# Kernel tuning notes

Measured on AMD Instinct MI355X. Metric: run time of the kernel, lower is better.

Reference implementation:

```python
import jax, jax.numpy as jnp
import numpy as np

N_NODES = 50000
N_EDGES = 800000
GEN_EPS = 1e-7
LN_EPS = 1e-5


def _mlp3_tanh(x, w0, b0, w1, b1, w2, b2):
    x = jnp.tanh(x @ w0.T + b0)
    x = jnp.tanh(x @ w1.T + b1)
    return jnp.tanh(x @ w2.T + b2)


def _gen_conv(x, src, dst, edge_attr, w0, b0, ln_w, ln_b, w1, b1):
    # GENConv(aggr='softmax', t=1): msg = relu(x_j + e) + eps
    msg = jax.nn.relu(x[src] + edge_attr) + GEN_EPS          # [E, 64]
    m = jax.ops.segment_max(msg, dst, num_segments=N_NODES)  # [N, 64]
    ex = jnp.exp(msg - m[dst])
    den = jax.ops.segment_sum(ex, dst, num_segments=N_NODES)
    alpha = ex / den[dst]                                    # scatter-softmax per dst
    agg = jax.ops.segment_sum(alpha * msg, dst, num_segments=N_NODES)
    h = x + agg                                              # x_r + aggregated messages
    # internal MLP: Linear(64->128), LayerNorm(128), ReLU, Linear(128->64)
    h = h @ w0.T + b0
    mu = jnp.mean(h, axis=-1, keepdims=True)
    var = jnp.mean((h - mu) ** 2, axis=-1, keepdims=True)
    h = ln_w * (h - mu) * jax.lax.rsqrt(var + LN_EPS) + ln_b
    h = jax.nn.relu(h)
    return h @ w1.T + b1


def setup_inputs() -> dict:
    key = jax.random.key(0)
    ks = jax.random.split(key, 32)
    s = 0.05
    d = {
        'node_features': jax.random.normal(ks[0], (N_NODES, 11), jnp.float32),
        'edge_features': jax.random.normal(ks[1], (N_EDGES, 3), jnp.float32),
        'edge_index': jax.random.randint(ks[2], (2, N_EDGES), 0, N_NODES, jnp.int32),
        'ne_w0': jax.random.normal(ks[3], (64, 11)) * s, 'ne_b0': jnp.zeros((64,)),
        'ne_w1': jax.random.normal(ks[4], (64, 64)) * s, 'ne_b1': jnp.zeros((64,)),
        'ne_w2': jax.random.normal(ks[5], (64, 64)) * s, 'ne_b2': jnp.zeros((64,)),
        'ee_w0': jax.random.normal(ks[6], (64, 3)) * s, 'ee_b0': jnp.zeros((64,)),
        'ee_w1': jax.random.normal(ks[7], (64, 64)) * s, 'ee_b1': jnp.zeros((64,)),
        'ee_w2': jax.random.normal(ks[8], (64, 64)) * s, 'ee_b2': jnp.zeros((64,)),
        'mp_w0': jax.random.normal(ks[9], (3, 128, 64)) * s,
        'mp_b0': jnp.zeros((3, 128)),
        'mp_ln_w': jnp.ones((3, 128)), 'mp_ln_b': jnp.zeros((3, 128)),
        'mp_w1': jax.random.normal(ks[10], (3, 64, 128)) * s,
        'mp_b1': jnp.zeros((3, 64)),
        'pi_w0': jax.random.normal(ks[11], (64, 64)) * s, 'pi_b0': jnp.zeros((64,)),
        'pi_w1': jax.random.normal(ks[12], (64, 64)) * s, 'pi_b1': jnp.zeros((64,)),
        'pi_w2': jax.random.normal(ks[13], (2, 64)) * s, 'pi_b2': jnp.zeros((2,)),
    }
    return {k: (v.astype(jnp.float32) if v.dtype != jnp.int32 else v) for k, v in d.items()}


def reference(node_features, edge_features, edge_index,
              ne_w0, ne_b0, ne_w1, ne_b1, ne_w2, ne_b2,
              ee_w0, ee_b0, ee_w1, ee_b1, ee_w2, ee_b2,
              mp_w0, mp_b0, mp_ln_w, mp_ln_b, mp_w1, mp_b1,
              pi_w0, pi_b0, pi_w1, pi_b1, pi_w2, pi_b2):
    src, dst = edge_index[0], edge_index[1]
    x = _mlp3_tanh(node_features, ne_w0, ne_b0, ne_w1, ne_b1, ne_w2, ne_b2)
    e = _mlp3_tanh(edge_features, ee_w0, ee_b0, ee_w1, ee_b1, ee_w2, ee_b2)
    for i in range(3):
        x = _gen_conv(x, src, dst, e, mp_w0[i], mp_b0[i], mp_ln_w[i], mp_ln_b[i], mp_w1[i], mp_b1[i])
    h = jnp.tanh(x @ pi_w0.T + pi_b0)
    h = jnp.tanh(h @ pi_w1.T + pi_b1)
    out = h @ pi_w2.T + pi_b2                 # [N, 2]
    # output.t().reshape(-1)[:n_turbines] == first column of out
    means = -30.0 + (out[:, 0] + 1.0) * 60.0 / 2.0
    return means
```

## Files before the change

kernel.cpp:

```cpp
#include <hip/hip_runtime.h>
#include <stdint.h>

#define N_NODES 50000
#define N_EDGES 800000

typedef unsigned short u16;
typedef unsigned int u32;
typedef __attribute__((ext_vector_type(8))) short short8;
typedef __attribute__((ext_vector_type(4))) float f32x4;
typedef __attribute__((ext_vector_type(4))) u32 u32x4;
typedef __attribute__((ext_vector_type(2))) u32 u32x2;

#define WAVE_SYNC() asm volatile("s_waitcnt lgkmcnt(0)" ::: "memory")

__device__ __forceinline__ float b2f(u16 v) {
    u32 u = ((u32)v) << 16; float f; __builtin_memcpy(&f, &u, 4); return f;
}
__device__ __forceinline__ u16 f2b(float f) {
    u32 u; __builtin_memcpy(&u, &f, 4);
    return (u16)((u + 0x8000u) >> 16);
}
__device__ __forceinline__ float lo2f(u32 p) {
    u32 u = p << 16; float f; __builtin_memcpy(&f, &u, 4); return f;
}
__device__ __forceinline__ float hi2f(u32 p) {
    u32 u = p & 0xffff0000u; float f; __builtin_memcpy(&f, &u, 4); return f;
}
__device__ __forceinline__ u32 pack2(float a, float b) {
    u32 ua, ub; __builtin_memcpy(&ua, &a, 4); __builtin_memcpy(&ub, &b, 4);
    return __builtin_amdgcn_perm(ub + 0x8000u, ua + 0x8000u, 0x07060302u);
}
__device__ __forceinline__ f32x4 mfma16(short8 a, short8 b, f32x4 c) {
    return __builtin_amdgcn_mfma_f32_16x16x32_bf16(a, b, c, 0, 0, 0);
}

#define TANH_TBL_N 192
__device__ __forceinline__ void build_tanh_tbl(float2* tbl) {
    int i = (int)threadIdx.x;
    if (i < TANH_TBL_N) {
        float x0 = i * 0.03125f, x1 = x0 + 0.03125f;
        float t0 = tanhf(x0), t1 = tanhf(x1);
        float s = (t1 - t0) * 32.f;
        tbl[i] = make_float2(fmaf(-s, x0, t0), s);
    }
    __syncthreads();
}
__device__ __forceinline__ float lut_tanh(const float2* __restrict__ tbl, float x) {
    float a = __builtin_fabsf(x);
    a = fminf(a, 5.96875f);
    int i = (int)(a * 32.f);
    float2 bs = tbl[i];
    float y = fmaf(bs.y, a, bs.x);
    return copysignf(y, x);
}

enum : int {
    NE_T0 = 0,     NE_B0 = 704,   NE_T1 = 768,   NE_B1 = 4864,  NE_T2 = 4928,  NE_B2 = 9024,
    EE_T0 = 9088,  EE_B0 = 9280,  EE_T1 = 9344,  EE_B1 = 13440, EE_T2 = 13504, EE_B2 = 17600,
    MP_T0 = 17664, MP_B0 = 42240, LNW_O = 42624, LNB_O = 43008, MP_T1 = 43392, MP_B1 = 67968,
    PI_T0 = 68160, PI_B0 = 72256, PI_T1 = 72320, PI_B1 = 76416, PI_W2 = 76480, PI_B2 = 76608,
    W_TOTAL = 76610
};

enum : int {
    FR_EE1 = 0, FR_EE2 = 4, FR_EE3 = 12, FR_NE1 = 20, FR_NE2 = 24, FR_NE3 = 32,
    FR_MP0 = 40, FR_MP1 = 88, FR_PI0 = 136, FR_PI1 = 144, FR_TOTAL = 152
};

#define OFF_W       ((size_t)0)
#define OFF_FLAG    ((size_t)0x60000)
#define OFF_WB      ((size_t)0x61000)
#define OFF_XB0     ((size_t)0x90000)
#define OFF_XB1     ((size_t)0x700000)
#define OFF_H64B    ((size_t)0xE00000)
#define OFF_E       ((size_t)0x1500000)
#define OFF_ROWPTR  ((size_t)0x8300000)
#define OFF_CURSOR  ((size_t)0x8340000)
#define OFF_CNT     ((size_t)0x8380000)
#define OFF_PERM    ((size_t)0x83C0000)
#define OFF_SRCS    ((size_t)0x8700000)
#define OFF_BSUM    ((size_t)0x8A80000)

struct Ptrs24 { const void* p[24]; };


__global__ void detect_kernel(const void* nf, int* flag) {
    u32 w = ((const u32*)nf)[threadIdx.x & 63];
    u32 lo = w & 0xffffu;
    int e = (int)((lo >> 7) & 0xff);
    int good = ((e >= 118 && e <= 132) || lo == 0) ? 1 : 0;
    unsigned long long b = __ballot(good != 0);
    if (threadIdx.x == 0) *flag = (__popcll(b) >= 48) ? 1 : 0;
}

__global__ void convert_weights(Ptrs24 ps, float* __restrict__ W, const int* flag) {
    const int segIN[24] = {11,64,64,64,64,64, 3,64,64,64,64,64, 64,384,384,384,128,192, 64,64,64,64,128,2};
    const int segOUT[24]= {64, 1,64, 1,64, 1, 64, 1,64, 1,64, 1, 128, 1,  1,  1, 64,  1, 64, 1,64, 1,  1,1};
    const int segS[24]  = { 1, 1, 1, 1, 1, 1,  1, 1, 1, 1, 1, 1,   3, 1,  1,  1,  3,  1,  1, 1, 1, 1,  1,1};
    const int segTR[24] = { 1, 0, 1, 0, 1, 0,  1, 0, 1, 0, 1, 0,   1, 0,  0,  0,  1,  0,  1, 0, 1, 0,  0,0};
    int t = blockIdx.x * blockDim.x + threadIdx.x;
    if (t >= W_TOTAL) return;
    bool bf = (*flag != 0);
    int seg = 0, off = t;
    for (;;) {
        int cnt = segIN[seg] * segOUT[seg] * segS[seg];
        if (off < cnt) break;
        off -= cnt; seg++;
    }
    int srcIdx;
    if (segTR[seg]) {
        int per = segIN[seg] * segOUT[seg];
        int s = off / per, d = off % per;
        int j = d / segOUT[seg], i = d % segOUT[seg];
        srcIdx = s * per + i * segIN[seg] + j;
    } else {
        srcIdx = off;
    }
    const void* p = ps.p[seg];
    W[t] = bf ? b2f(((const u16*)p)[srcIdx]) : ((const float*)p)[srcIdx];
}

__global__ void make_frags(const float* __restrict__ W, u16* __restrict__ Wb) {
    const int base[15] = {FR_EE1,FR_EE2,FR_EE3,FR_NE1,FR_NE2,FR_NE3,
                          FR_MP0,FR_MP0+16,FR_MP0+32, FR_MP1,FR_MP1+16,FR_MP1+32,
                          FR_PI0,FR_PI1,FR_TOTAL};
    const int woff[14] = {EE_T0,EE_T1,EE_T2, NE_T0,NE_T1,NE_T2,
                          MP_T0,MP_T0+8192,MP_T0+16384, MP_T1,MP_T1+8192,MP_T1+16384,
                          PI_T0,PI_T1};
    const int kreal[14] = {3,64,64, 11,64,64, 64,64,64, 128,128,128, 64,64};
    const int nn[14]    = {64,64,64, 64,64,64, 128,128,128, 64,64,64, 64,64};
    int t = blockIdx.x * blockDim.x + threadIdx.x;
    if (t >= FR_TOTAL * 512) return;
    int f = t >> 9, r = t & 511, lane = r >> 3, j = r & 7;
    int l = 0;
    while (f >= base[l + 1]) l++;
    int lf = f - base[l];
    int NT = nn[l] >> 4;
    int kt = lf / NT, nt = lf % NT;
    int k = kt * 32 + (lane >> 4) * 8 + j;
    int n = nt * 16 + (lane & 15);
    float v = (k < kreal[l]) ? W[woff[l] + k * nn[l] + n] : 0.f;
    u32 u; __builtin_memcpy(&u, &v, 4);
    Wb[t] = (u16)((u + 0x7fffu + ((u >> 16) & 1u)) >> 16);
}


__global__ void hist_kernel(const int* __restrict__ dst, int* __restrict__ cnts) {
    int e = blockIdx.x * blockDim.x + threadIdx.x;
    if (e < N_EDGES) atomicAdd(&cnts[dst[e]], 1);
}

__global__ void scanA(const int* __restrict__ cnts, int* __restrict__ prow,
                      int* __restrict__ bsum) {
    __shared__ int wsum[16];
    int tid = threadIdx.x, lane = tid & 63, wid = tid >> 6;
    int i0 = blockIdx.x * 2048 + tid * 2;
    int v0 = 0, v1 = 0;
    if (i0 >= 1 && i0 <= N_NODES) v0 = (cnts[i0 - 1] + 1) & ~1;
    if (i0 + 1 <= N_NODES && i0 + 1 >= 1) v1 = (cnts[i0] + 1) & ~1;
    int v = v0 + v1;
#pragma unroll
    for (int off = 1; off < 64; off <<= 1) {
        int t = __shfl_up(v, off, 64);
        if (lane >= off) v += t;
    }
    if (lane == 63) wsum[wid] = v;
    __syncthreads();
    if (tid == 0) { int a = 0; for (int w = 0; w < 16; w++) { a += wsum[w]; wsum[w] = a; } }
    __syncthreads();
    int incl = v + (wid ? wsum[wid - 1] : 0);
    if (i0 <= N_NODES) prow[i0] = incl - v1;
    if (i0 + 1 <= N_NODES) prow[i0 + 1] = incl;
    if (tid == 1023) bsum[blockIdx.x] = incl;
}
__global__ void scanB(int* __restrict__ bsum, int nb) {
    int lane = threadIdx.x;
    int v = (lane < nb) ? bsum[lane] : 0;
#pragma unroll
    for (int off = 1; off < 64; off <<= 1) {
        int t = __shfl_up(v, off, 64);
        if (lane >= off) v += t;
    }
    if (lane < nb) bsum[lane] = v;
}
__global__ void scanC(const int* __restrict__ bsum, int* __restrict__ prow,
                      int* __restrict__ cursor) {
    int i = blockIdx.x * 1024 + threadIdx.x;
    if (i > N_NODES) return;
    int b = i >> 11;
    int v = prow[i] + (b ? bsum[b - 1] : 0);
    prow[i] = v;
    if (i < N_NODES) cursor[i] = v;
}

__global__ void scatter_kernel(const int* __restrict__ dst, const int* __restrict__ src,
                               int* __restrict__ cursor, int* __restrict__ perm,
                               int* __restrict__ srcs) {
    int e = blockIdx.x * blockDim.x + threadIdx.x;
    if (e >= N_EDGES) return;
    int p = atomicAdd(&cursor[dst[e]], 1);
    perm[e] = p;
    srcs[p] = src[e];
}


template<int KT, int NT, int INSTR>
__device__ __forceinline__ void mfma_layer(const u32* ldsin, int lane,
        const short8* __restrict__ Wf, int basef, const float* __restrict__ bias, f32x4* acc) {
    int q = lane >> 4, mr = lane & 15;
#pragma unroll
    for (int nt = 0; nt < NT; nt++) acc[nt] = *(const f32x4*)(bias + nt * 16 + q * 4);
#pragma unroll
    for (int kt = 0; kt < KT; kt++) {
        short8 act = *(const short8*)(ldsin + mr * INSTR + kt * 16 + q * 4);
#pragma unroll
        for (int nt = 0; nt < NT; nt++)
            acc[nt] = mfma16(Wf[(basef + kt * NT + nt) * 64 + lane], act, acc[nt]);
    }
}

template<int KT, int NT>
__device__ __forceinline__ void mfma_layer_reg(const short8* act, int lane,
        const short8* __restrict__ Wf, int basef, const float* __restrict__ bias, f32x4* acc) {
    int q = lane >> 4;
#pragma unroll
    for (int nt = 0; nt < NT; nt++) acc[nt] = *(const f32x4*)(bias + nt * 16 + q * 4);
#pragma unroll
    for (int kt = 0; kt < KT; kt++)
#pragma unroll
        for (int nt = 0; nt < NT; nt++)
            acc[nt] = mfma16(Wf[(basef + kt * NT + nt) * 64 + lane], act[kt], acc[nt]);
}

template<int NT, int OUTSTR>
__device__ __forceinline__ void tanh_pack_lds(const f32x4* acc, u32* ldsout, int lane,
                                              const float2* __restrict__ tbl) {
    int q = lane >> 4, mr = lane & 15;
#pragma unroll
    for (int nt = 0; nt < NT; nt++) {
        f32x4 a = acc[nt];
        ldsout[mr * OUTSTR + nt * 8 + q * 2 + 0] = pack2(lut_tanh(tbl, a[0]), lut_tanh(tbl, a[1]));
        ldsout[mr * OUTSTR + nt * 8 + q * 2 + 1] = pack2(lut_tanh(tbl, a[2]), lut_tanh(tbl, a[3]));
    }
}


__global__ __launch_bounds__(256) void edge_encoder(const void* ef, u32* __restrict__ ebuf,
        const int* __restrict__ perm, const float* __restrict__ W,
        const short8* __restrict__ Wf, const int* flag) {
    __shared__ u32 lds[4 * 1152];
    __shared__ float2 tbl[TANH_TBL_N];
    build_tanh_tbl(tbl);
    int wv = threadIdx.x >> 6, lane = threadIdx.x & 63;
    u32* B0 = lds + wv * 1152;
    u32* B1 = B0 + 576;
    long ebase = (long)blockIdx.x * 64 + wv * 16;
    bool bf = (*flag != 0);
    if (lane < 16) {
        long e = ebase + lane;
        float i0, i1, i2;
        if (bf) { const u16* p = (const u16*)ef + e * 3; i0 = b2f(p[0]); i1 = b2f(p[1]); i2 = b2f(p[2]); }
        else    { const float* p = (const float*)ef + e * 3; i0 = p[0]; i1 = p[1]; i2 = p[2]; }
        u32* row = B0 + lane * 36;
        row[0] = pack2(i0, i1); row[1] = pack2(i2, 0.f);
#pragma unroll
        for (int d = 2; d < 16; d++) row[d] = 0;
    }
    WAVE_SYNC();
    f32x4 acc[4];
    mfma_layer<1, 4, 36>(B0, lane, Wf, FR_EE1, W + EE_B0, acc);
    tanh_pack_lds<4, 36>(acc, B1, lane, tbl);
    WAVE_SYNC();
    mfma_layer<2, 4, 36>(B1, lane, Wf, FR_EE2, W + EE_B1, acc);
    tanh_pack_lds<4, 36>(acc, B0, lane, tbl);
    WAVE_SYNC();
    mfma_layer<2, 4, 36>(B0, lane, Wf, FR_EE3, W + EE_B2, acc);
    tanh_pack_lds<4, 36>(acc, B1, lane, tbl);
    WAVE_SYNC();
    int ro = lane >> 2, cc = (lane & 3) * 8;
    long e = ebase + ro;
    long prowp = perm[e];
    u32x4 v0 = *(const u32x4*)&B1[ro * 36 + cc];
    u32x4 v1 = *(const u32x4*)&B1[ro * 36 + cc + 4];
    *(u32x4*)&ebuf[prowp * 32 + cc] = v0;
    *(u32x4*)&ebuf[prowp * 32 + cc + 4] = v1;
}

__global__ __launch_bounds__(256) void node_encoder(const void* nf,
        u16* __restrict__ xbf, const float* __restrict__ W,
        const short8* __restrict__ Wf, const int* flag) {
    __shared__ u32 lds[4 * 1152];
    __shared__ float2 tbl[TANH_TBL_N];
    build_tanh_tbl(tbl);
    int wv = threadIdx.x >> 6, lane = threadIdx.x & 63;
    int q = lane >> 4, mr = lane & 15;
    u32* B0 = lds + wv * 1152;
    u32* B1 = B0 + 576;
    long nbase = (long)blockIdx.x * 64 + wv * 16;
    bool bf = (*flag != 0);
    if (lane < 16) {
        long n = nbase + lane;
        float in[12];
#pragma unroll
        for (int j = 0; j < 12; j++) in[j] = 0.f;
        if (n < N_NODES) {
#pragma unroll
            for (int j = 0; j < 11; j++)
                in[j] = bf ? b2f(((const u16*)nf)[n * 11 + j]) : ((const float*)nf)[n * 11 + j];
        }
        u32* row = B0 + lane * 36;
#pragma unroll
        for (int d = 0; d < 6; d++) row[d] = pack2(in[2 * d], in[2 * d + 1]);
#pragma unroll
        for (int d = 6; d < 16; d++) row[d] = 0;
    }
    WAVE_SYNC();
    f32x4 acc[4];
    mfma_layer<1, 4, 36>(B0, lane, Wf, FR_NE1, W + NE_B0, acc);
    tanh_pack_lds<4, 36>(acc, B1, lane, tbl);
    WAVE_SYNC();
    mfma_layer<2, 4, 36>(B1, lane, Wf, FR_NE2, W + NE_B1, acc);
    tanh_pack_lds<4, 36>(acc, B0, lane, tbl);
    WAVE_SYNC();
    mfma_layer<2, 4, 36>(B0, lane, Wf, FR_NE3, W + NE_B2, acc);
    long n = nbase + mr;
    if (n < N_NODES) {
#pragma unroll
        for (int nt = 0; nt < 4; nt++) {
            float v0 = lut_tanh(tbl, acc[nt][0]), v1 = lut_tanh(tbl, acc[nt][1]);
            float v2 = lut_tanh(tbl, acc[nt][2]), v3 = lut_tanh(tbl, acc[nt][3]);
            u32x2 pb; pb.x = pack2(v0, v1); pb.y = pack2(v2, v3);
            *(u32x2*)&xbf[n * 64 + nt * 16 + q * 4] = pb;
        }
    }
}

__global__ __launch_bounds__(256) void aggregate_kernel(
        const u32* __restrict__ xbf32, const u32* __restrict__ ebuf32,
        const int* __restrict__ srcs, const int* __restrict__ prow,
        u32* __restrict__ h64bf32) {
    int wid = (int)((blockIdx.x * 256 + threadIdx.x) >> 6);
    int lane = (int)(threadIdx.x & 63);
    int n0 = __builtin_amdgcn_readfirstlane(wid) * 4;
    if (n0 >= N_NODES) return;
    int half = lane >> 5, h = lane & 31;
    int rl = n0 + (lane < 4 ? lane : 4);
    if (rl > N_NODES) rl = N_NODES;
    int rv = prow[rl];
    int win = __shfl(rv, 0, 64);
    int sk = srcs[win + lane];
    for (int j = 0; j < 4; j++) {
        int n = n0 + j;
        if (n >= N_NODES) break;
        int kb = __shfl(rv, j, 64);
        int ke = __shfl(rv, j + 1, 64);
        u32 xr = xbf32[(long)n * 32 + h];
        float num0 = 0.f, den0 = 0.f, num1 = 0.f, den1 = 0.f;
        for (int k = kb; k < ke; k += 2) {
            if (k + 1 >= win + 64) { win = k; sk = srcs[win + lane]; }
            int s = __shfl(sk, k - win + half, 64);
            u32 ev = ebuf32[(long)(k + half) * 32 + h];
            bool valid = s >= 0;
            long sr = valid ? (long)s : 0;
            u32 xv = xbf32[sr * 32 + h];
            float m0 = fmaxf(lo2f(xv) + lo2f(ev), 0.f) + 1e-7f;
            float m1 = fmaxf(hi2f(xv) + hi2f(ev), 0.f) + 1e-7f;
            float w0 = valid ? __expf(m0) : 0.f;
            float w1 = valid ? __expf(m1) : 0.f;
            num0 = fmaf(w0, m0, num0); den0 += w0;
            num1 = fmaf(w1, m1, num1); den1 += w1;
        }
        num0 += __shfl_xor(num0, 32, 64); den0 += __shfl_xor(den0, 32, 64);
        num1 += __shfl_xor(num1, 32, 64); den1 += __shfl_xor(den1, 32, 64);
        if (half == 0) {
            float agg0 = (den0 > 0.f) ? __fdividef(num0, den0) : 0.f;
            float agg1 = (den1 > 0.f) ? __fdividef(num1, den1) : 0.f;
            h64bf32[(long)n * 32 + h] = pack2(lo2f(xr) + agg0, hi2f(xr) + agg1);
        }
    }
}

__global__ __launch_bounds__(256) void mlp_fused(const u16* __restrict__ h64bf,
        u16* __restrict__ xbf,
        const float* __restrict__ W, const short8* __restrict__ Wf, int r) {
    __shared__ u32 lds[4 * 1088];
    int wv = threadIdx.x >> 6, lane = threadIdx.x & 63;
    int q = lane >> 4, mr = lane & 15;
    u32* bufY = lds + wv * 1088;
    long nbase = (long)blockIdx.x * 64 + wv * 16;
    long row = nbase + mr;
    long rc = (row < N_NODES) ? row : (N_NODES - 1);
    short8 act[2];
#pragma unroll
    for (int kt = 0; kt < 2; kt++)
        act[kt] = *(const short8*)&h64bf[rc * 64 + kt * 32 + q * 8];
    f32x4 acc[8];
    mfma_layer_reg<2, 8>(act, lane, Wf, FR_MP0 + r * 16, W + MP_B0 + r * 128, acc);
    float s = 0.f, sq = 0.f;
#pragma unroll
    for (int nt = 0; nt < 8; nt++)
#pragma unroll
        for (int rr = 0; rr < 4; rr++) { float v = acc[nt][rr]; s += v; sq = fmaf(v, v, sq); }
    s += __shfl_xor(s, 16, 64);  s += __shfl_xor(s, 32, 64);
    sq += __shfl_xor(sq, 16, 64); sq += __shfl_xor(sq, 32, 64);
    float mu = s * (1.f / 128.f);
    float var = sq * (1.f / 128.f) - mu * mu;
    float inv = rsqrtf(var + 1e-5f);
    const float* LW = W + LNW_O + r * 128;
    const float* LB = W + LNB_O + r * 128;
#pragma unroll
    for (int nt = 0; nt < 8; nt++) {
        f32x4 lw = *(const f32x4*)(LW + nt * 16 + q * 4);
        f32x4 lb = *(const f32x4*)(LB + nt * 16 + q * 4);
        float u0 = fmaxf(fmaf((acc[nt][0] - mu) * inv, lw[0], lb[0]), 0.f);
        float u1 = fmaxf(fmaf((acc[nt][1] - mu) * inv, lw[1], lb[1]), 0.f);
        float u2 = fmaxf(fmaf((acc[nt][2] - mu) * inv, lw[2], lb[2]), 0.f);
        float u3 = fmaxf(fmaf((acc[nt][3] - mu) * inv, lw[3], lb[3]), 0.f);
        bufY[mr * 68 + nt * 8 + q * 2 + 0] = pack2(u0, u1);
        bufY[mr * 68 + nt * 8 + q * 2 + 1] = pack2(u2, u3);
    }
    WAVE_SYNC();
    f32x4 acc2[4];
    mfma_layer<4, 4, 68>(bufY, lane, Wf, FR_MP1 + r * 16, W + MP_B1 + r * 64, acc2);
    if (row < N_NODES) {
#pragma unroll
        for (int nt = 0; nt < 4; nt++) {
            f32x4 v = acc2[nt];
            u32x2 pb; pb.x = pack2(v[0], v[1]); pb.y = pack2(v[2], v[3]);
            *(u32x2*)&xbf[row * 64 + nt * 16 + q * 4] = pb;
        }
    }
}

__global__ __launch_bounds__(256) void policy_head(const u16* __restrict__ xbf, void* out,
        const float* __restrict__ W, const short8* __restrict__ Wf, const int* flag) {
    __shared__ u32 lds[4 * 576];
    __shared__ float2 tbl[TANH_TBL_N];
    build_tanh_tbl(tbl);
    int wv = threadIdx.x >> 6, lane = threadIdx.x & 63;
    int q = lane >> 4, mr = lane & 15;
    u32* bufY = lds + wv * 576;
    long nbase = (long)blockIdx.x * 64 + wv * 16;
    long row = nbase + mr;
    long rc = (row < N_NODES) ? row : (N_NODES - 1);
    bool bf = (*flag != 0);
    short8 act[2];
#pragma unroll
    for (int kt = 0; kt < 2; kt++)
        act[kt] = *(const short8*)&xbf[rc * 64 + kt * 32 + q * 8];
    f32x4 acc[4];
    mfma_layer_reg<2, 4>(act, lane, Wf, FR_PI0, W + PI_B0, acc);
    tanh_pack_lds<4, 36>(acc, bufY, lane, tbl);
    WAVE_SYNC();
    mfma_layer<2, 4, 36>(bufY, lane, Wf, FR_PI1, W + PI_B1, acc);
    float o = 0.f;
#pragma unroll
    for (int nt = 0; nt < 4; nt++) {
        f32x4 w2 = *(const f32x4*)(W + PI_W2 + nt * 16 + q * 4);
#pragma unroll
        for (int rr = 0; rr < 4; rr++) o = fmaf(lut_tanh(tbl, acc[nt][rr]), w2[rr], o);
    }
    o += __shfl_xor(o, 16, 64);
    o += __shfl_xor(o, 32, 64);
    if (lane < 16 && row < N_NODES) {
        float means = 30.f * (o + W[PI_B2]);
        if (bf) ((u16*)out)[row] = f2b(means);
        else    ((float*)out)[row] = means;
    }
}

extern "C" void kernel_launch(void* const* d_in, const int* in_sizes, int n_in,
                              void* d_out, int out_size, void* d_ws, size_t ws_size,
                              hipStream_t stream) {
    char* ws = (char*)d_ws;
    float* W      = (float*)(ws + OFF_W);
    int*   flag   = (int*)(ws + OFF_FLAG);
    u16*   Wb     = (u16*)(ws + OFF_WB);
    const short8* Wf = (const short8*)(ws + OFF_WB);
    u16*   xb0    = (u16*)(ws + OFF_XB0);
    u16*   xb1    = (u16*)(ws + OFF_XB1);
    u16*   h64bf  = (u16*)(ws + OFF_H64B);
    u32*   h64b32 = (u32*)(ws + OFF_H64B);
    u32*   ebuf32 = (u32*)(ws + OFF_E);
    int*   prow   = (int*)(ws + OFF_ROWPTR);
    int*   cursor = (int*)(ws + OFF_CURSOR);
    int*   cnts   = (int*)(ws + OFF_CNT);
    int*   perm   = (int*)(ws + OFF_PERM);
    int*   srcs   = (int*)(ws + OFF_SRCS);
    int*   bsum   = (int*)(ws + OFF_BSUM);

    const int* ei   = (const int*)d_in[2];
    const int* srcv = ei;
    const int* dstv = ei + N_EDGES;

    detect_kernel<<<1, 64, 0, stream>>>(d_in[0], flag);
    hipMemsetAsync(cnts, 0, N_NODES * sizeof(int), stream);
    hipMemsetAsync(srcs, 0xFF, (size_t)0x340000, stream);

    Ptrs24 ps;
    for (int k = 0; k < 24; k++) ps.p[k] = d_in[3 + k];
    convert_weights<<<(W_TOTAL + 255) / 256, 256, 0, stream>>>(ps, W, flag);
    make_frags<<<(FR_TOTAL * 512 + 255) / 256, 256, 0, stream>>>(W, Wb);

    hist_kernel<<<(N_EDGES + 255) / 256, 256, 0, stream>>>(dstv, cnts);
    scanA<<<25, 1024, 0, stream>>>(cnts, prow, bsum);
    scanB<<<1, 64, 0, stream>>>(bsum, 25);
    scanC<<<(N_NODES + 1024) / 1024, 1024, 0, stream>>>(bsum, prow, cursor);
    scatter_kernel<<<(N_EDGES + 255) / 256, 256, 0, stream>>>(dstv, srcv, cursor, perm, srcs);

    node_encoder<<<(N_NODES + 63) / 64, 256, 0, stream>>>(d_in[0], xb0, W, Wf, flag);
    edge_encoder<<<N_EDGES / 64, 256, 0, stream>>>(d_in[1], ebuf32, perm, W, Wf, flag);

    u16* xbc = xb0; u16* xbn = xb1;
    const int aggBlocks = ((N_NODES + 3) / 4 * 64 + 255) / 256;
    for (int r = 0; r < 3; r++) {
        aggregate_kernel<<<aggBlocks, 256, 0, stream>>>(
            (const u32*)xbc, ebuf32, srcs, prow, h64b32);
        mlp_fused<<<(N_NODES + 63) / 64, 256, 0, stream>>>(h64bf, xbn, W, Wf, r);
        u16* tb = xbc; xbc = xbn; xbn = tb;
    }
    policy_head<<<(N_NODES + 63) / 64, 256, 0, stream>>>(xbc, d_out, W, Wf, flag);
}
```

Baseline: 461.9 us.

## Restructure aggregation to two nodes per wave; precompute tanh table once; drop scanB

Each aggregate wave now handles 2 destination nodes instead of 4. It stages 64-edge windows of source indices in LDS and walks a shared window for both nodes, instead of reloading a register window and shuffling. The tanh lookup table is now built once in make_frags and copied into LDS by each kernel, so blocks no longer call tanhf. scanB is removed by having scanC sum the preceding block totals in a loop, and encoder LDS zeroing is spread across all lanes. These target per-node serialisation, launch count and redundant transcendental work. In exchange there are more waves for aggregation and extra LDS syncs.

After: 431.9 us. -6.5%, faster.

```diff
diff --git a/kernel.cpp b/kernel.cpp
--- a/kernel.cpp
+++ b/kernel.cpp
@@ -35,14 +35,9 @@
 }
 
 #define TANH_TBL_N 192
-__device__ __forceinline__ void build_tanh_tbl(float2* tbl) {
+__device__ __forceinline__ void load_tbl(const float2* __restrict__ g, float2* tbl) {
     int i = (int)threadIdx.x;
-    if (i < TANH_TBL_N) {
-        float x0 = i * 0.03125f, x1 = x0 + 0.03125f;
-        float t0 = tanhf(x0), t1 = tanhf(x1);
-        float s = (t1 - t0) * 32.f;
-        tbl[i] = make_float2(fmaf(-s, x0, t0), s);
-    }
+    if (i < TANH_TBL_N) tbl[i] = g[i];
     __syncthreads();
 }
 __device__ __forceinline__ float lut_tanh(const float2* __restrict__ tbl, float x) {
@@ -70,6 +65,7 @@
 #define OFF_W       ((size_t)0)
 #define OFF_FLAG    ((size_t)0x60000)
 #define OFF_WB      ((size_t)0x61000)
+#define OFF_TBL     ((size_t)0x88000)
 #define OFF_XB0     ((size_t)0x90000)
 #define OFF_XB1     ((size_t)0x700000)
 #define OFF_H64B    ((size_t)0xE00000)
@@ -120,7 +116,8 @@
     W[t] = bf ? b2f(((const u16*)p)[srcIdx]) : ((const float*)p)[srcIdx];
 }
 
-__global__ void make_frags(const float* __restrict__ W, u16* __restrict__ Wb) {
+__global__ void make_frags(const float* __restrict__ W, u16* __restrict__ Wb,
+                           float2* __restrict__ gtbl) {
     const int base[15] = {FR_EE1,FR_EE2,FR_EE3,FR_NE1,FR_NE2,FR_NE3,
                           FR_MP0,FR_MP0+16,FR_MP0+32, FR_MP1,FR_MP1+16,FR_MP1+32,
                           FR_PI0,FR_PI1,FR_TOTAL};
@@ -130,7 +127,16 @@
     const int kreal[14] = {3,64,64, 11,64,64, 64,64,64, 128,128,128, 64,64};
     const int nn[14]    = {64,64,64, 64,64,64, 128,128,128, 64,64,64, 64,64};
     int t = blockIdx.x * blockDim.x + threadIdx.x;
-    if (t >= FR_TOTAL * 512) return;
+    if (t >= FR_TOTAL * 512) {
+        int i = t - FR_TOTAL * 512;
+        if (i < TANH_TBL_N) {
+            float x0 = i * 0.03125f, x1 = x0 + 0.03125f;
+            float t0 = tanhf(x0), t1 = tanhf(x1);
+            float s = (t1 - t0) * 32.f;
+            gtbl[i] = make_float2(fmaf(-s, x0, t0), s);
+        }
+        return;
+    }
     int f = t >> 9, r = t & 511, lane = r >> 3, j = r & 7;
     int l = 0;
     while (f >= base[l + 1]) l++;
@@ -173,22 +179,14 @@
     if (i0 + 1 <= N_NODES) prow[i0 + 1] = incl;
     if (tid == 1023) bsum[blockIdx.x] = incl;
 }
-__global__ void scanB(int* __restrict__ bsum, int nb) {
-    int lane = threadIdx.x;
-    int v = (lane < nb) ? bsum[lane] : 0;
-#pragma unroll
-    for (int off = 1; off < 64; off <<= 1) {
-        int t = __shfl_up(v, off, 64);
-        if (lane >= off) v += t;
-    }
-    if (lane < nb) bsum[lane] = v;
-}
 __global__ void scanC(const int* __restrict__ bsum, int* __restrict__ prow,
                       int* __restrict__ cursor) {
     int i = blockIdx.x * 1024 + threadIdx.x;
     if (i > N_NODES) return;
-    int b = i >> 11;
-    int v = prow[i] + (b ? bsum[b - 1] : 0);
+    int nb = (int)(blockIdx.x >> 1);
+    int add = 0;
+    for (int b = 0; b < nb; b++) add += bsum[b];
+    int v = prow[i] + add;
     prow[i] = v;
     if (i < N_NODES) cursor[i] = v;
 }
@@ -244,18 +242,27 @@
     }
 }
 
+__device__ __forceinline__ void zero_stage(u32* B0, int lane) {
+#pragma unroll
+    for (int it = 0; it < 4; it++) {
+        int f = lane + 64 * it;
+        B0[(f >> 4) * 36 + (f & 15)] = 0;
+    }
+}
+
 
 __global__ __launch_bounds__(256) void edge_encoder(const void* ef, u32* __restrict__ ebuf,
         const int* __restrict__ perm, const float* __restrict__ W,
-        const short8* __restrict__ Wf, const int* flag) {
+        const short8* __restrict__ Wf, const float2* __restrict__ gtbl, const int* flag) {
     __shared__ u32 lds[4 * 1152];
     __shared__ float2 tbl[TANH_TBL_N];
-    build_tanh_tbl(tbl);
+    load_tbl(gtbl, tbl);
     int wv = threadIdx.x >> 6, lane = threadIdx.x & 63;
     u32* B0 = lds + wv * 1152;
     u32* B1 = B0 + 576;
     long ebase = (long)blockIdx.x * 64 + wv * 16;
     bool bf = (*flag != 0);
+    zero_stage(B0, lane);
     if (lane < 16) {
         long e = ebase + lane;
         float i0, i1, i2;
@@ -263,8 +270,6 @@
         else    { const float* p = (const float*)ef + e * 3; i0 = p[0]; i1 = p[1]; i2 = p[2]; }
         u32* row = B0 + lane * 36;
         row[0] = pack2(i0, i1); row[1] = pack2(i2, 0.f);
-#pragma unroll
-        for (int d = 2; d < 16; d++) row[d] = 0;
     }
     WAVE_SYNC();
     f32x4 acc[4];
@@ -288,31 +293,29 @@
 
 __global__ __launch_bounds__(256) void node_encoder(const void* nf,
         u16* __restrict__ xbf, const float* __restrict__ W,
-        const short8* __restrict__ Wf, const int* flag) {
+        const short8* __restrict__ Wf, const float2* __restrict__ gtbl, const int* flag) {
     __shared__ u32 lds[4 * 1152];
     __shared__ float2 tbl[TANH_TBL_N];
-    build_tanh_tbl(tbl);
+    load_tbl(gtbl, tbl);
     int wv = threadIdx.x >> 6, lane = threadIdx.x & 63;
     int q = lane >> 4, mr = lane & 15;
     u32* B0 = lds + wv * 1152;
     u32* B1 = B0 + 576;
     long nbase = (long)blockIdx.x * 64 + wv * 16;
     bool bf = (*flag != 0);
+    zero_stage(B0, lane);
     if (lane < 16) {
         long n = nbase + lane;
-        float in[12];
-#pragma unroll
-        for (int j = 0; j < 12; j++) in[j] = 0.f;
         if (n < N_NODES) {
+            float in[11];
 #pragma unroll
             for (int j = 0; j < 11; j++)
                 in[j] = bf ? b2f(((const u16*)nf)[n * 11 + j]) : ((const float*)nf)[n * 11 + j];
-        }
-        u32* row = B0 + lane * 36;
-#pragma unroll
-        for (int d = 0; d < 6; d++) row[d] = pack2(in[2 * d], in[2 * d + 1]);
-#pragma unroll
-        for (int d = 6; d < 16; d++) row[d] = 0;
+            u32* row = B0 + lane * 36;
+#pragma unroll
+            for (int d = 0; d < 5; d++) row[d] = pack2(in[2 * d], in[2 * d + 1]);
+            row[5] = pack2(in[10], 0.f);
+        }
     }
     WAVE_SYNC();
     f32x4 acc[4];
@@ -339,43 +342,65 @@
         const u32* __restrict__ xbf32, const u32* __restrict__ ebuf32,
         const int* __restrict__ srcs, const int* __restrict__ prow,
         u32* __restrict__ h64bf32) {
+    __shared__ int ldsW[4][64];
+    int wv = threadIdx.x >> 6;
     int wid = (int)((blockIdx.x * 256 + threadIdx.x) >> 6);
     int lane = (int)(threadIdx.x & 63);
-    int n0 = __builtin_amdgcn_readfirstlane(wid) * 4;
+    int n0 = __builtin_amdgcn_readfirstlane(wid) * 2;
     if (n0 >= N_NODES) return;
     int half = lane >> 5, h = lane & 31;
-    int rl = n0 + (lane < 4 ? lane : 4);
-    if (rl > N_NODES) rl = N_NODES;
+    int rl = n0 + (lane < 2 ? lane : 2);
     int rv = prow[rl];
-    int win = __shfl(rv, 0, 64);
-    int sk = srcs[win + lane];
-    for (int j = 0; j < 4; j++) {
-        int n = n0 + j;
-        if (n >= N_NODES) break;
-        int kb = __shfl(rv, j, 64);
-        int ke = __shfl(rv, j + 1, 64);
-        u32 xr = xbf32[(long)n * 32 + h];
-        float num0 = 0.f, den0 = 0.f, num1 = 0.f, den1 = 0.f;
-        for (int k = kb; k < ke; k += 2) {
-            if (k + 1 >= win + 64) { win = k; sk = srcs[win + lane]; }
-            int s = __shfl(sk, k - win + half, 64);
-            u32 ev = ebuf32[(long)(k + half) * 32 + h];
-            bool valid = s >= 0;
-            long sr = valid ? (long)s : 0;
-            u32 xv = xbf32[sr * 32 + h];
+    int kb0 = __shfl(rv, 0, 64);
+    int kb1 = __shfl(rv, 1, 64);
+    int kb2 = __shfl(rv, 2, 64);
+    float num[2][2], den[2][2];
+#pragma unroll
+    for (int j = 0; j < 2; j++) { num[j][0] = num[j][1] = den[j][0] = den[j][1] = 0.f; }
+    for (int wb = kb0; wb < kb2; wb += 64) {
+        ldsW[wv][lane] = srcs[wb + lane];
+        WAVE_SYNC();
+        int we = wb + 64;
+        int hi0 = kb1 < we ? kb1 : we;
+        int lo1 = kb1 > wb ? kb1 : wb;
+        int hi1 = kb2 < we ? kb2 : we;
+#pragma unroll 2
+        for (int k = wb; k < hi0; k += 2) {
+            int s = ldsW[wv][k - wb + half];
+            u32 ev = ebuf32[(size_t)(k + half) * 32 + h];
+            u32 xv = xbf32[(size_t)(s > 0 ? s : 0) * 32 + h];
             float m0 = fmaxf(lo2f(xv) + lo2f(ev), 0.f) + 1e-7f;
             float m1 = fmaxf(hi2f(xv) + hi2f(ev), 0.f) + 1e-7f;
-            float w0 = valid ? __expf(m0) : 0.f;
-            float w1 = valid ? __expf(m1) : 0.f;
-            num0 = fmaf(w0, m0, num0); den0 += w0;
-            num1 = fmaf(w1, m1, num1); den1 += w1;
-        }
-        num0 += __shfl_xor(num0, 32, 64); den0 += __shfl_xor(den0, 32, 64);
-        num1 += __shfl_xor(num1, 32, 64); den1 += __shfl_xor(den1, 32, 64);
+            float w0 = __expf(m0), w1 = __expf(m1);
+            if (s < 0) { w0 = 0.f; w1 = 0.f; }
+            num[0][0] = fmaf(w0, m0, num[0][0]); den[0][0] += w0;
+            num[0][1] = fmaf(w1, m1, num[0][1]); den[0][1] += w1;
+        }
+#pragma unroll 2
+        for (int k = lo1; k < hi1; k += 2) {
+            int s = ldsW[wv][k - wb + half];
+            u32 ev = ebuf32[(size_t)(k + half) * 32 + h];
+            u32 xv = xbf32[(size_t)(s > 0 ? s : 0) * 32 + h];
+            float m0 = fmaxf(lo2f(xv) + lo2f(ev), 0.f) + 1e-7f;
+            float m1 = fmaxf(hi2f(xv) + hi2f(ev), 0.f) + 1e-7f;
+            float w0 = __expf(m0), w1 = __expf(m1);
+            if (s < 0) { w0 = 0.f; w1 = 0.f; }
+            num[1][0] = fmaf(w0, m0, num[1][0]); den[1][0] += w0;
+            num[1][1] = fmaf(w1, m1, num[1][1]); den[1][1] += w1;
+        }
+        WAVE_SYNC();
+    }
+#pragma unroll
+    for (int j = 0; j < 2; j++) {
+        float n0f = num[j][0] + __shfl_xor(num[j][0], 32, 64);
+        float d0f = den[j][0] + __shfl_xor(den[j][0], 32, 64);
+        float n1f = num[j][1] + __shfl_xor(num[j][1], 32, 64);
+        float d1f = den[j][1] + __shfl_xor(den[j][1], 32, 64);
         if (half == 0) {
-            float agg0 = (den0 > 0.f) ? __fdividef(num0, den0) : 0.f;
-            float agg1 = (den1 > 0.f) ? __fdividef(num1, den1) : 0.f;
-            h64bf32[(long)n * 32 + h] = pack2(lo2f(xr) + agg0, hi2f(xr) + agg1);
+            float agg0 = (d0f > 0.f) ? __fdividef(n0f, d0f) : 0.f;
+            float agg1 = (d1f > 0.f) ? __fdividef(n1f, d1f) : 0.f;
+            u32 xr = xbf32[(size_t)(n0 + j) * 32 + h];
+            h64bf32[(size_t)(n0 + j) * 32 + h] = pack2(lo2f(xr) + agg0, hi2f(xr) + agg1);
         }
     }
 }
@@ -433,10 +458,11 @@
 }
 
 __global__ __launch_bounds__(256) void policy_head(const u16* __restrict__ xbf, void* out,
-        const float* __restrict__ W, const short8* __restrict__ Wf, const int* flag) {
+        const float* __restrict__ W, const short8* __restrict__ Wf,
+        const float2* __restrict__ gtbl, const int* flag) {
     __shared__ u32 lds[4 * 576];
     __shared__ float2 tbl[TANH_TBL_N];
-    build_tanh_tbl(tbl);
+    load_tbl(gtbl, tbl);
     int wv = threadIdx.x >> 6, lane = threadIdx.x & 63;
     int q = lane >> 4, mr = lane & 15;
     u32* bufY = lds + wv * 576;
@@ -477,6 +503,7 @@
     int*   flag   = (int*)(ws + OFF_FLAG);
     u16*   Wb     = (u16*)(ws + OFF_WB);
     const short8* Wf = (const short8*)(ws + OFF_WB);
+    float2* gtbl  = (float2*)(ws + OFF_TBL);
     u16*   xb0    = (u16*)(ws + OFF_XB0);
     u16*   xb1    = (u16*)(ws + OFF_XB1);
     u16*   h64bf  = (u16*)(ws + OFF_H64B);
@@ -500,24 +527,23 @@
     Ptrs24 ps;
     for (int k = 0; k < 24; k++) ps.p[k] = d_in[3 + k];
     convert_weights<<<(W_TOTAL + 255) / 256, 256, 0, stream>>>(ps, W, flag);
-    make_frags<<<(FR_TOTAL * 512 + 255) / 256, 256, 0, stream>>>(W, Wb);
+    make_frags<<<(FR_TOTAL * 512 + TANH_TBL_N + 255) / 256, 256, 0, stream>>>(W, Wb, gtbl);
 
     hist_kernel<<<(N_EDGES + 255) / 256, 256, 0, stream>>>(dstv, cnts);
     scanA<<<25, 1024, 0, stream>>>(cnts, prow, bsum);
-    scanB<<<1, 64, 0, stream>>>(bsum, 25);
     scanC<<<(N_NODES + 1024) / 1024, 1024, 0, stream>>>(bsum, prow, cursor);
     scatter_kernel<<<(N_EDGES + 255) / 256, 256, 0, stream>>>(dstv, srcv, cursor, perm, srcs);
 
-    node_encoder<<<(N_NODES + 63) / 64, 256, 0, stream>>>(d_in[0], xb0, W, Wf, flag);
-    edge_encoder<<<N_EDGES / 64, 256, 0, stream>>>(d_in[1], ebuf32, perm, W, Wf, flag);
+    node_encoder<<<(N_NODES + 63) / 64, 256, 0, stream>>>(d_in[0], xb0, W, Wf, gtbl, flag);
+    edge_encoder<<<N_EDGES / 64, 256, 0, stream>>>(d_in[1], ebuf32, perm, W, Wf, gtbl, flag);
 
     u16* xbc = xb0; u16* xbn = xb1;
-    const int aggBlocks = ((N_NODES + 3) / 4 * 64 + 255) / 256;
+    const int aggBlocks = (N_NODES / 2 * 64) / 256;
     for (int r = 0; r < 3; r++) {
         aggregate_kernel<<<aggBlocks, 256, 0, stream>>>(
             (const u32*)xbc, ebuf32, srcs, prow, h64b32);
         mlp_fused<<<(N_NODES + 63) / 64, 256, 0, stream>>>(h64bf, xbn, W, Wf, r);
         u16* tb = xbc; xbc = xbn; xbn = tb;
     }
-    policy_head<<<(N_NODES + 63) / 64, 256, 0, stream>>>(xbc, d_out, W, Wf, flag);
-}
+    policy_head<<<(N_NODES + 63) / 64, 256, 0, stream>>>(xbc, d_out, W, Wf, gtbl, flag);
+}
```
